# Kernel optimization log

Hardware: AMD Instinct MI355X
Metric: run time of the kernel (lower is better)

The kernel has to match this reference:

```python
import jax, jax.numpy as jnp
import numpy as np

BINS = 10
LOSS_WEIGHT = 1.0


def setup_inputs() -> dict:
    key = jax.random.key(0)
    k1, k2, k3 = jax.random.split(key, 3)
    N, C = 262144, 80
    pred = jax.random.normal(k1, (N, C), dtype=jnp.float32)
    # binary class targets (sparse positives, as in detection)
    target = (jax.random.uniform(k2, (N, C)) < 0.02).astype(jnp.float32)
    # 1 = valid sample, 0 = ignored
    label_weight = (jax.random.uniform(k3, (N, C)) < 0.95).astype(jnp.float32)
    return {"pred": pred, "target": target, "label_weight": label_weight}


def reference(pred, target, label_weight):
    # GHM-C loss, momentum=0 path (no EMA buffer).
    valid = label_weight > 0
    validf = valid.astype(jnp.float32)
    tot = jnp.maximum(jnp.sum(validf), 1.0)

    # gradient norm g = |sigmoid(pred).detach() - target|, in [0, 1]
    g = jnp.abs(jax.lax.stop_gradient(jax.nn.sigmoid(pred)) - target)
    # edges are i/BINS with last edge 1+1e-6, so bin i covers [i/B, (i+1)/B);
    # equivalent to floor(g*B) clipped to [0, B-1] (g==1 lands in last bin).
    bin_idx = jnp.clip(jnp.floor(g * BINS).astype(jnp.int32), 0, BINS - 1)

    # per-bin counts over valid elements (single-pass histogram)
    counts = jax.ops.segment_sum(validf.reshape(-1), bin_idx.reshape(-1),
                                 num_segments=BINS)
    n = jnp.sum(counts > 0).astype(jnp.float32)  # number of non-empty bins
    per_bin_w = jnp.where(counts > 0, tot / jnp.maximum(counts, 1.0), 0.0)
    weights = per_bin_w[bin_idx] * validf  # scattered weight assignment
    weights = jnp.where(n > 0, weights / n, weights)

    # binary_cross_entropy_with_logits, elementwise: softplus(x) - x*t
    bce = jax.nn.softplus(pred) - pred * target
    loss = jnp.sum(bce * weights) / tot
    return loss * LOSS_WEIGHT
```

## Files before the change

kernel.cpp:

```cpp
#include <hip/hip_runtime.h>

#define BINS 10


__global__ __launch_bounds__(64) void ghmc_zero(float* ws_sum, int* ws_cnt) {
    int i = threadIdx.x;
    if (i < BINS) { ws_sum[i] = 0.0f; ws_cnt[i] = 0; }
}

__device__ __forceinline__ void ghmc_elem(float pk, float tk, float wk,
                                          float lsum[BINS], int lcnt[BINS]) {
    if (wk > 0.0f) {
        float e = __expf(-fabsf(pk));
        float r = 1.0f / (1.0f + e);
        float s = (pk >= 0.0f) ? r : (1.0f - r);
        float g = fabsf(s - tk);
        int bin = (int)(g * 10.0f);
        bin = bin > (BINS - 1) ? (BINS - 1) : bin;
        float bce = fmaxf(pk, 0.0f) + log1pf(e) - pk * tk;
#pragma unroll
        for (int b = 0; b < BINS; ++b) {
            if (bin == b) { lsum[b] += bce; lcnt[b] += 1; }
        }
    }
}

__global__ __launch_bounds__(256) void ghmc_main(
    const float* __restrict__ pred, const float* __restrict__ targ,
    const float* __restrict__ lw,
    float* __restrict__ ws_sum, int* __restrict__ ws_cnt, int n) {

    float lsum[BINS];
    int   lcnt[BINS];
#pragma unroll
    for (int b = 0; b < BINS; ++b) { lsum[b] = 0.0f; lcnt[b] = 0; }

    const int tid    = blockIdx.x * blockDim.x + threadIdx.x;
    const int stride = gridDim.x * blockDim.x;
    const int nvec   = n >> 2;

    const float4* p4 = (const float4*)pred;
    const float4* t4 = (const float4*)targ;
    const float4* w4 = (const float4*)lw;

    for (int i = tid; i < nvec; i += stride) {
        float4 p = p4[i], t = t4[i], w = w4[i];
        const float* pp = (const float*)&p;
        const float* tt = (const float*)&t;
        const float* ww = (const float*)&w;
#pragma unroll
        for (int k = 0; k < 4; ++k)
            ghmc_elem(pp[k], tt[k], ww[k], lsum, lcnt);
    }
    {
        int rem = n & 3;
        if (tid < rem) {
            int i = (nvec << 2) + tid;
            ghmc_elem(pred[i], targ[i], lw[i], lsum, lcnt);
        }
    }

    __shared__ float s_sum[BINS];
    __shared__ int   s_cnt[BINS];
    if (threadIdx.x < BINS) { s_sum[threadIdx.x] = 0.0f; s_cnt[threadIdx.x] = 0; }
    __syncthreads();

    const int lane = threadIdx.x & 63;
#pragma unroll
    for (int b = 0; b < BINS; ++b) {
        float s = lsum[b];
        int   c = lcnt[b];
#pragma unroll
        for (int off = 32; off > 0; off >>= 1) {
            s += __shfl_xor(s, off, 64);
            c += __shfl_xor(c, off, 64);
        }
        if (lane == 0) {
            atomicAdd(&s_sum[b], s);
            atomicAdd(&s_cnt[b], c);
        }
    }
    __syncthreads();

    if (threadIdx.x < BINS) {
        float s = s_sum[threadIdx.x];
        int   c = s_cnt[threadIdx.x];
        if (c != 0) {
            atomicAdd(&ws_sum[threadIdx.x], s);
            atomicAdd(&ws_cnt[threadIdx.x], c);
        }
    }
}

__global__ __launch_bounds__(64) void ghmc_finalize(
    const float* __restrict__ ws_sum, const int* __restrict__ ws_cnt,
    float* __restrict__ out) {
    if (threadIdx.x == 0) {
        float acc = 0.0f;
        int n = 0;
        for (int b = 0; b < BINS; ++b) {
            int c = ws_cnt[b];
            if (c > 0) { n += 1; acc += ws_sum[b] / (float)c; }
        }
        out[0] = (n > 0) ? (acc / (float)n) : 0.0f;
    }
}

extern "C" void kernel_launch(void* const* d_in, const int* in_sizes, int n_in,
                              void* d_out, int out_size, void* d_ws, size_t ws_size,
                              hipStream_t stream) {
    const float* pred = (const float*)d_in[0];
    const float* targ = (const float*)d_in[1];
    const float* lw   = (const float*)d_in[2];
    float* out = (float*)d_out;
    const int n = in_sizes[0];

    float* ws_sum = (float*)d_ws;
    int*   ws_cnt = (int*)((char*)d_ws + BINS * sizeof(float));

    ghmc_zero<<<1, 64, 0, stream>>>(ws_sum, ws_cnt);

    const int threads = 256;
    const int blocks  = 2048;
    ghmc_main<<<blocks, threads, 0, stream>>>(pred, targ, lw, ws_sum, ws_cnt, n);

    ghmc_finalize<<<1, 64, 0, stream>>>(ws_sum, ws_cnt, out);
}
```

Measured before the change: 277.4 us.

## Accumulate histogram via per-wave shared-memory atomics and use fast rcp/log2

Replaces the per-thread register histogram (10 predicated adds per element plus a shuffle reduction) with per-wave shared-memory bins updated by LDS atomics for every element. It also swaps the reciprocal and log1pf for the hardware rcp and log2 intrinsics. The aim is to cut per-element predicated work and register pressure. The cost is that every valid element now issues two LDS atomics to only 10 addresses, which risks heavy same-address contention.

```diff
diff --git a/kernel.cpp b/kernel.cpp
--- a/kernel.cpp
+++ b/kernel.cpp
@@ -1,6 +1,7 @@
 #include <hip/hip_runtime.h>
 
 #define BINS 10
+#define WPB 4
 
 
 __global__ __launch_bounds__(64) void ghmc_zero(float* ws_sum, int* ws_cnt) {
@@ -9,19 +10,18 @@
 }
 
 __device__ __forceinline__ void ghmc_elem(float pk, float tk, float wk,
-                                          float lsum[BINS], int lcnt[BINS]) {
+                                          float* wsum, int* wcnt) {
     if (wk > 0.0f) {
-        float e = __expf(-fabsf(pk));
-        float r = 1.0f / (1.0f + e);
-        float s = (pk >= 0.0f) ? r : (1.0f - r);
-        float g = fabsf(s - tk);
+        float e    = __expf(-fabsf(pk));
+        float onep = 1.0f + e;
+        float r    = __builtin_amdgcn_rcpf(onep);
+        float s    = (pk >= 0.0f) ? r : (1.0f - r);
+        float g    = fabsf(s - tk);
         int bin = (int)(g * 10.0f);
         bin = bin > (BINS - 1) ? (BINS - 1) : bin;
-        float bce = fmaxf(pk, 0.0f) + log1pf(e) - pk * tk;
-#pragma unroll
-        for (int b = 0; b < BINS; ++b) {
-            if (bin == b) { lsum[b] += bce; lcnt[b] += 1; }
-        }
+        float bce = fmaxf(pk, 0.0f) - pk * tk + 0.69314718056f * __log2f(onep);
+        atomicAdd(&wsum[bin], bce);
+        atomicAdd(&wcnt[bin], 1);
     }
 }
 
@@ -30,10 +30,17 @@
     const float* __restrict__ lw,
     float* __restrict__ ws_sum, int* __restrict__ ws_cnt, int n) {
 
-    float lsum[BINS];
-    int   lcnt[BINS];
-#pragma unroll
-    for (int b = 0; b < BINS; ++b) { lsum[b] = 0.0f; lcnt[b] = 0; }
+    __shared__ float s_sum[WPB][BINS];
+    __shared__ int   s_cnt[WPB][BINS];
+    if (threadIdx.x < WPB * BINS) {
+        ((float*)s_sum)[threadIdx.x] = 0.0f;
+        ((int*)s_cnt)[threadIdx.x]   = 0;
+    }
+    __syncthreads();
+
+    const int wave = threadIdx.x >> 6;
+    float* wsum = s_sum[wave];
+    int*   wcnt = s_cnt[wave];
 
     const int tid    = blockIdx.x * blockDim.x + threadIdx.x;
     const int stride = gridDim.x * blockDim.x;
@@ -50,41 +57,26 @@
         const float* ww = (const float*)&w;
 #pragma unroll
         for (int k = 0; k < 4; ++k)
-            ghmc_elem(pp[k], tt[k], ww[k], lsum, lcnt);
+            ghmc_elem(pp[k], tt[k], ww[k], wsum, wcnt);
     }
     {
         int rem = n & 3;
         if (tid < rem) {
             int i = (nvec << 2) + tid;
-            ghmc_elem(pred[i], targ[i], lw[i], lsum, lcnt);
+            ghmc_elem(pred[i], targ[i], lw[i], wsum, wcnt);
         }
     }
 
-    __shared__ float s_sum[BINS];
-    __shared__ int   s_cnt[BINS];
-    if (threadIdx.x < BINS) { s_sum[threadIdx.x] = 0.0f; s_cnt[threadIdx.x] = 0; }
-    __syncthreads();
-
-    const int lane = threadIdx.x & 63;
-#pragma unroll
-    for (int b = 0; b < BINS; ++b) {
-        float s = lsum[b];
-        int   c = lcnt[b];
-#pragma unroll
-        for (int off = 32; off > 0; off >>= 1) {
-            s += __shfl_xor(s, off, 64);
-            c += __shfl_xor(c, off, 64);
-        }
-        if (lane == 0) {
-            atomicAdd(&s_sum[b], s);
-            atomicAdd(&s_cnt[b], c);
-        }
-    }
     __syncthreads();
 
     if (threadIdx.x < BINS) {
-        float s = s_sum[threadIdx.x];
-        int   c = s_cnt[threadIdx.x];
+        float s = 0.0f;
+        int   c = 0;
+#pragma unroll
+        for (int wv = 0; wv < WPB; ++wv) {
+            s += s_sum[wv][threadIdx.x];
+            c += s_cnt[wv][threadIdx.x];
+        }
         if (c != 0) {
             atomicAdd(&ws_sum[threadIdx.x], s);
             atomicAdd(&ws_cnt[threadIdx.x], c);
```

Result: no change. 280.4 us (+1.1%).
